# Performance work log

Hardware: AMD Instinct MI355X
Metric: run time of the kernel (lower is better)

The kernel has to match this reference:

```python
import jax, jax.numpy as jnp
import numpy as np

B, T, C = 2, 2048, 1024
H = 16
D = C // H
SCALE = 0.1 / (D ** 0.5)  # nonstandard 0.1/sqrt(head_dim) scale from source


def setup_inputs() -> dict:
    key = jax.random.key(0)
    ks = jax.random.split(key, 5)
    s = 0.02
    return {
        "x": jax.random.normal(ks[0], (B, T, C), jnp.float32),
        "w_attn": jax.random.normal(ks[1], (C, 3 * C), jnp.float32) * s,
        "b_attn": jax.random.normal(ks[2], (3 * C,), jnp.float32) * s,
        "w_proj": jax.random.normal(ks[3], (C, C), jnp.float32) * s,
        "b_proj": jax.random.normal(ks[4], (C,), jnp.float32) * s,
    }


def reference(x, w_attn, b_attn, w_proj, b_proj):
    Bs, Ts, Cs = x.shape
    qkv = x @ w_attn + b_attn                      # [B,T,3C]
    q, k, v = jnp.split(qkv, 3, axis=-1)
    q = q.reshape(Bs, Ts, H, D)                    # [B,T,H,D]
    k = k.reshape(Bs, Ts, H, D)
    v = v.reshape(Bs, Ts, H, D)
    attn = jnp.einsum("bthd,bshd->bhts", q, k) * SCALE  # [B,H,T,T]
    causal = jnp.tril(jnp.ones((Ts, Ts), dtype=bool))
    attn = jnp.where(causal, attn, -jnp.inf)
    attn = jax.nn.softmax(attn, axis=-1)
    y = jnp.einsum("bhts,bshd->bthd", attn, v).reshape(Bs, Ts, Cs)
    return y @ w_proj + b_proj
```

## Files before the change

### kernel.cpp

```cpp
#include <hip/hip_runtime.h>


#define Bz 2
#define Tz 2048
#define Cz 1024
#define Hz 16
#define Dz 64
#define QSCALE 0.01803368801111437f

typedef unsigned short u16;
typedef short bf16x4 __attribute__((ext_vector_type(4)));
typedef short bf16x8 __attribute__((ext_vector_type(8)));
typedef float f32x4 __attribute__((ext_vector_type(4)));

#define MFMA32(A, B, C) __builtin_amdgcn_mfma_f32_16x16x32_bf16(A, B, C, 0, 0, 0)

__device__ inline f32x4 mfma16(bf16x4 a, bf16x4 b, f32x4 c) {
#if defined(__HIP_DEVICE_COMPILE__)
  return __builtin_amdgcn_mfma_f32_16x16x16bf16_1k(a, b, c, 0, 0, 0);
#else
  return c;
#endif
}

__device__ inline u16 f2bf(float f) {
  return (u16)((__float_as_uint(f) + 0x8000u) >> 16);
}

__device__ inline float fexp2(float x) {
#if __has_builtin(__builtin_amdgcn_exp2f)
  return __builtin_amdgcn_exp2f(x);
#else
  return exp2f(x);
#endif
}

__device__ inline void gl_lds16(const u16* g, u16* l) {
  __builtin_amdgcn_global_load_lds(
      (const __attribute__((address_space(1))) void*)g,
      (__attribute__((address_space(3))) void*)l, 16, 0, 0);
}

#define NCAST 4096
#define NTA   3072
__global__ __launch_bounds__(256) void prep_kernel(const float* __restrict__ x,
                                                   const float* __restrict__ wa,
                                                   const float* __restrict__ wp,
                                                   u16* __restrict__ xb,
                                                   u16* __restrict__ waT,
                                                   u16* __restrict__ wpT) {
  const int bx = blockIdx.x, t = threadIdx.x;
  if (bx < NCAST) {
    int i = bx * 256 + t;
    float4 v = ((const float4*)x)[i];
    ushort4 o = {f2bf(v.x), f2bf(v.y), f2bf(v.z), f2bf(v.w)};
    ((ushort4*)xb)[i] = o;
    return;
  }
  __shared__ float tile[32][33];
  const float* W;
  u16* WT;
  int N, idx;
  if (bx < NCAST + NTA) {
    W = wa; WT = waT; N = 3 * Cz; idx = bx - NCAST;
  } else {
    W = wp; WT = wpT; N = Cz; idx = bx - NCAST - NTA;
  }
  const int n0 = (idx % (N / 32)) * 32, k0 = (idx / (N / 32)) * 32;
  const int tx = t & 31, ty = t >> 5;
#pragma unroll
  for (int i = 0; i < 4; ++i)
    tile[ty + 8 * i][tx] = W[(size_t)(k0 + ty + 8 * i) * N + n0 + tx];
  __syncthreads();
#pragma unroll
  for (int i = 0; i < 4; ++i)
    WT[(size_t)(n0 + ty + 8 * i) * Cz + k0 + tx] = f2bf(tile[tx][ty + 8 * i]);
}

template <bool OUT_BF16, int TN>
__global__ __launch_bounds__(256) void gemm_bt(const u16* __restrict__ A,
                                               const u16* __restrict__ BT,
                                               const float* __restrict__ bias,
                                               void* __restrict__ Cout,
                                               int M, int N, int K,
                                               int qcols, float qscale) {
  __shared__ __align__(16) u16 As[128 * 64];
  __shared__ __align__(16) u16 Bs[TN * 64];
  constexpr int NT = TN / 32;
  const int t = threadIdx.x;
  const int wave = t >> 6, lane = t & 63;
  const int lm = lane & 15, lg = lane >> 4;
  const int wm = wave >> 1, wn = wave & 1;
  const int m0 = blockIdx.y * 128, n0 = blockIdx.x * TN;

  const int lrow = lane >> 3;
  const int gseg = (lane & 7) ^ lrow;
  const size_t a_base = (size_t)(m0 + 32 * wave + lrow) * K + gseg * 8;
  u16* const a_lds = &As[(32 * wave) * 64];
  const size_t b_base = (size_t)(n0 + (TN / 4) * wave + lrow) * K + gseg * 8;
  u16* const b_lds = &Bs[((TN / 4) * wave) * 64];

  f32x4 acc[4][NT];
#pragma unroll
  for (int mt = 0; mt < 4; ++mt)
#pragma unroll
    for (int nt = 0; nt < NT; ++nt)
#pragma unroll
      for (int i = 0; i < 4; ++i) acc[mt][nt][i] = 0.f;

  for (int k0 = 0; k0 < K; k0 += 64) {
    __syncthreads();
#pragma unroll
    for (int i = 0; i < 4; ++i)
      gl_lds16(A + a_base + (size_t)(8 * i) * K + k0, a_lds + i * 8 * 64);
#pragma unroll
    for (int i = 0; i < NT; ++i)
      gl_lds16(BT + b_base + (size_t)(8 * i) * K + k0, b_lds + i * 8 * 64);
    __syncthreads();

#pragma unroll
    for (int h = 0; h < 2; ++h) {
      const int rs = ((lg + 4 * h) ^ (lm & 7)) * 8;
      bf16x8 af[4], bfr[NT];
#pragma unroll
      for (int mt = 0; mt < 4; ++mt)
        af[mt] = *(const bf16x8*)&As[(64 * wm + 16 * mt + lm) * 64 + rs];
#pragma unroll
      for (int nt = 0; nt < NT; ++nt)
        bfr[nt] = *(const bf16x8*)&Bs[((TN / 2) * wn + 16 * nt + lm) * 64 + rs];
#pragma unroll
      for (int mt = 0; mt < 4; ++mt)
#pragma unroll
        for (int nt = 0; nt < NT; ++nt)
          acc[mt][nt] = MFMA32(af[mt], bfr[nt], acc[mt][nt]);
    }
  }

#pragma unroll
  for (int nt = 0; nt < NT; ++nt) {
    int gc = n0 + (TN / 2) * wn + 16 * nt + lm;
    float bv = bias[gc];
    float sc = (gc < qcols) ? qscale : 1.f;
#pragma unroll
    for (int mt = 0; mt < 4; ++mt) {
#pragma unroll
      for (int i = 0; i < 4; ++i) {
        int gr = m0 + 64 * wm + 16 * mt + 4 * lg + i;
        float v = (acc[mt][nt][i] + bv) * sc;
        if (OUT_BF16)
          ((u16*)Cout)[(size_t)gr * N + gc] = f2bf(v);
        else
          ((float*)Cout)[(size_t)gr * N + gc] = v;
      }
    }
  }
}

__global__ __launch_bounds__(256) void attn_kernel(const u16* __restrict__ qkv,
                                                   u16* __restrict__ yb) {
  __shared__ __align__(16) u16 Ks[64][72];
  __shared__ __align__(16) u16 Vt[64][72];

  const int t = threadIdx.x;
  const int wave = t >> 6, lane = t & 63;
  const int lm = lane & 15, lg = lane >> 4;
  const int kg8 = lg << 3;
  const int x = blockIdx.x;
  const int bh = x & 31, qtp = x >> 5;
  const int qt = (qtp < 16) ? qtp : 47 - qtp;
  const int b = bh >> 4, h = bh & 15;
  const int q0 = qt * 64;
  const size_t rowstride = 3 * Cz;
  const u16* qbase = qkv + (size_t)b * Tz * rowstride + h * Dz;

  bf16x8 qf[2];
  {
    const u16* qrow = qbase + (size_t)(q0 + wave * 16 + lm) * rowstride + kg8;
    qf[0] = *(const bf16x8*)qrow;
    qf[1] = *(const bf16x8*)(qrow + 32);
  }

  float psum = 0.f;
  f32x4 Oa[4];
#pragma unroll
  for (int i = 0; i < 4; ++i)
#pragma unroll
    for (int j = 0; j < 4; ++j) Oa[i][j] = 0.f;

  const int ksr = t >> 2, kds = (t & 3) << 4;
  const int vsp = t & 31, vds = (t >> 5) << 3;
  const u16* kbase = qbase + Cz + (size_t)ksr * rowstride + kds;
  const u16* vbase = qbase + 2 * Cz + (size_t)(2 * vsp) * rowstride + vds;
  const size_t tilestep = 64 * rowstride;

  uint4 krA[2], vrA[2], krB[2], vrB[2];
  {
    krA[0] = *(const uint4*)kbase;
    krA[1] = *(const uint4*)(kbase + 8);
    vrA[0] = *(const uint4*)vbase;
    vrA[1] = *(const uint4*)(vbase + rowstride);
    const size_t t1 = (qt >= 1) ? tilestep : 0;
    krB[0] = *(const uint4*)(kbase + t1);
    krB[1] = *(const uint4*)(kbase + t1 + 8);
    vrB[0] = *(const uint4*)(vbase + t1);
    vrB[1] = *(const uint4*)(vbase + t1 + rowstride);
  }

  auto stage = [&](uint4 (&kr)[2], uint4 (&vr)[2], int ktc) {
    __syncthreads();
    *(uint4*)&Ks[ksr][kds] = kr[0];
    *(uint4*)&Ks[ksr][kds + 8] = kr[1];
    {
      unsigned av[4] = {vr[0].x, vr[0].y, vr[0].z, vr[0].w};
      unsigned cv[4] = {vr[1].x, vr[1].y, vr[1].z, vr[1].w};
#pragma unroll
      for (int j = 0; j < 4; ++j) {
        unsigned w0 = (av[j] & 0xffffu) | (cv[j] << 16);
        unsigned w1 = (av[j] >> 16) | (cv[j] & 0xffff0000u);
        *(unsigned*)&Vt[vds + 2 * j][2 * vsp] = w0;
        *(unsigned*)&Vt[vds + 2 * j + 1][2 * vsp] = w1;
      }
    }
    __syncthreads();

    if (ktc + 2 <= qt) {
      const u16* kp = kbase + (size_t)(ktc + 2) * tilestep;
      const u16* vp = vbase + (size_t)(ktc + 2) * tilestep;
      kr[0] = *(const uint4*)kp;
      kr[1] = *(const uint4*)(kp + 8);
      vr[0] = *(const uint4*)vp;
      vr[1] = *(const uint4*)(vp + rowstride);
    }

    f32x4 S[4];
#pragma unroll
    for (int c = 0; c < 4; ++c) {
      bf16x8 k0 = *(const bf16x8*)&Ks[c * 16 + lm][kg8];
      bf16x8 k1 = *(const bf16x8*)&Ks[c * 16 + lm][32 + kg8];
      f32x4 s;
#pragma unroll
      for (int i = 0; i < 4; ++i) s[i] = 0.f;
      s = MFMA32(k0, qf[0], s);
      s = MFMA32(k1, qf[1], s);
      S[c] = s;
    }

    const bool diag = (ktc == qt);
    const int qloc = 16 * wave + lm;
    bf16x4 pf[4];
#pragma unroll
    for (int c = 0; c < 4; ++c) {
#pragma unroll
      for (int r = 0; r < 4; ++r) {
        float p = fexp2(S[c][r]);
        if (diag && (c * 16 + 4 * lg + r) > qloc) p = 0.f;
        psum += p;
        pf[c][r] = (short)f2bf(p);
      }
    }

#pragma unroll
    for (int dt = 0; dt < 4; ++dt) {
#pragma unroll
      for (int c = 0; c < 4; ++c) {
        bf16x4 vfr = *(const bf16x4*)&Vt[16 * dt + lm][c * 16 + 4 * lg];
        Oa[dt] = mfma16(pf[c], vfr, Oa[dt]);
      }
    }
  };

  for (int kt = 0; kt <= qt; kt += 2) {
    stage(krA, vrA, kt);
    if (kt + 1 <= qt) stage(krB, vrB, kt + 1);
  }

  float s = psum;
  s += __shfl_xor(s, 16);
  s += __shfl_xor(s, 32);
  const float linv = 1.f / s;
  float invq[4];
#pragma unroll
  for (int r = 0; r < 4; ++r)
    invq[r] = __shfl(linv, 20 * lg + r);
  __syncthreads();
#pragma unroll
  for (int dt = 0; dt < 4; ++dt)
#pragma unroll
    for (int r = 0; r < 4; ++r)
      Ks[16 * wave + 4 * lg + r][16 * dt + lm] = f2bf(Oa[dt][r] * invq[r]);
  __syncthreads();
  {
    const int row = lane >> 2, seg = lane & 3;
    const uint4* src = (const uint4*)&Ks[16 * wave + row][seg * 16];
    uint4 v0 = src[0];
    uint4 v1 = src[1];
    u16* dst = yb + (size_t)(b * Tz + q0 + 16 * wave + row) * Cz + h * Dz + seg * 16;
    *(uint4*)dst = v0;
    *(uint4*)(dst + 8) = v1;
  }
}

extern "C" void kernel_launch(void* const* d_in, const int* in_sizes, int n_in,
                              void* d_out, int out_size, void* d_ws, size_t ws_size,
                              hipStream_t stream) {
  const float* x      = (const float*)d_in[0];
  const float* w_attn = (const float*)d_in[1];
  const float* b_attn = (const float*)d_in[2];
  const float* w_proj = (const float*)d_in[3];
  const float* b_proj = (const float*)d_in[4];

  char* ws = (char*)d_ws;
  u16* xb   = (u16*)(ws);
  u16* waT  = (u16*)(ws + (8ull << 20));
  u16* wpT  = (u16*)(ws + (14ull << 20));
  u16* qkvb = (u16*)(ws + (16ull << 20));
  u16* yb   = (u16*)(ws + (40ull << 20));

  const int M = Bz * Tz;

  prep_kernel<<<NCAST + NTA + 1024, 256, 0, stream>>>(x, w_attn, w_proj, xb, waT, wpT);
  gemm_bt<true, 128><<<dim3(3 * Cz / 128, M / 128), 256, 0, stream>>>(
      xb, waT, b_attn, qkvb, M, 3 * Cz, Cz, Cz, QSCALE);
  attn_kernel<<<1024, 256, 0, stream>>>(qkvb, yb);
  gemm_bt<false, 64><<<dim3(Cz / 64, M / 128), 256, 0, stream>>>(
      yb, wpT, b_proj, d_out, M, Cz, Cz, 0, 1.f);
}
```

Before: 207.9 us.

## Double-buffer K/V shared tiles to halve barriers per attention tile

The attention kernel now keeps two LDS buffers for K and transposed V. Each iteration writes the next tile into the idle buffer while computing on the current one, so it needs one barrier per tile instead of two, and global prefetch runs two tiles ahead from a single register set. The LDS row paddings also change (76 and 74 elements) to alter bank mapping. Those strides are no longer 16-byte multiples, so the vector LDS reads and writes become misaligned, which could add cost or depend on unaligned-LDS support.

```diff
diff --git a/kernel.cpp b/kernel.cpp
--- a/kernel.cpp
+++ b/kernel.cpp
@@ -7,6 +7,8 @@
 #define Hz 16
 #define Dz 64
 #define QSCALE 0.01803368801111437f
+#define KSS 76
+#define VTS 74
 
 typedef unsigned short u16;
 typedef short bf16x4 __attribute__((ext_vector_type(4)));
@@ -158,8 +160,8 @@
 
 __global__ __launch_bounds__(256) void attn_kernel(const u16* __restrict__ qkv,
                                                    u16* __restrict__ yb) {
-  __shared__ __align__(16) u16 Ks[64][72];
-  __shared__ __align__(16) u16 Vt[64][72];
+  __shared__ __align__(16) u16 Ks[2][64][KSS];
+  __shared__ __align__(16) u16 Vt[2][64][VTS];
 
   const int t = threadIdx.x;
   const int wave = t >> 6, lane = t & 63;
@@ -193,50 +195,46 @@
   const u16* vbase = qbase + 2 * Cz + (size_t)(2 * vsp) * rowstride + vds;
   const size_t tilestep = 64 * rowstride;
 
-  uint4 krA[2], vrA[2], krB[2], vrB[2];
-  {
-    krA[0] = *(const uint4*)kbase;
-    krA[1] = *(const uint4*)(kbase + 8);
-    vrA[0] = *(const uint4*)vbase;
-    vrA[1] = *(const uint4*)(vbase + rowstride);
-    const size_t t1 = (qt >= 1) ? tilestep : 0;
-    krB[0] = *(const uint4*)(kbase + t1);
-    krB[1] = *(const uint4*)(kbase + t1 + 8);
-    vrB[0] = *(const uint4*)(vbase + t1);
-    vrB[1] = *(const uint4*)(vbase + t1 + rowstride);
-  }
-
-  auto stage = [&](uint4 (&kr)[2], uint4 (&vr)[2], int ktc) {
+  uint4 kr[2], vr[2];
+  auto load_tile = [&](int kt) {
+    const u16* kp = kbase + (size_t)kt * tilestep;
+    const u16* vp = vbase + (size_t)kt * tilestep;
+    kr[0] = *(const uint4*)kp;
+    kr[1] = *(const uint4*)(kp + 8);
+    vr[0] = *(const uint4*)vp;
+    vr[1] = *(const uint4*)(vp + rowstride);
+  };
+  auto stage_write = [&](int buf) {
+    *(uint4*)&Ks[buf][ksr][kds] = kr[0];
+    *(uint4*)&Ks[buf][ksr][kds + 8] = kr[1];
+    unsigned av[4] = {vr[0].x, vr[0].y, vr[0].z, vr[0].w};
+    unsigned cv[4] = {vr[1].x, vr[1].y, vr[1].z, vr[1].w};
+#pragma unroll
+    for (int j = 0; j < 4; ++j) {
+      unsigned w0 = (av[j] & 0xffffu) | (cv[j] << 16);
+      unsigned w1 = (av[j] >> 16) | (cv[j] & 0xffff0000u);
+      *(unsigned*)&Vt[buf][vds + 2 * j][2 * vsp] = w0;
+      *(unsigned*)&Vt[buf][vds + 2 * j + 1][2 * vsp] = w1;
+    }
+  };
+
+  load_tile(0);
+  stage_write(0);
+  load_tile(1);
+
+  for (int kt = 0; kt <= qt; ++kt) {
     __syncthreads();
-    *(uint4*)&Ks[ksr][kds] = kr[0];
-    *(uint4*)&Ks[ksr][kds + 8] = kr[1];
-    {
-      unsigned av[4] = {vr[0].x, vr[0].y, vr[0].z, vr[0].w};
-      unsigned cv[4] = {vr[1].x, vr[1].y, vr[1].z, vr[1].w};
-#pragma unroll
-      for (int j = 0; j < 4; ++j) {
-        unsigned w0 = (av[j] & 0xffffu) | (cv[j] << 16);
-        unsigned w1 = (av[j] >> 16) | (cv[j] & 0xffff0000u);
-        *(unsigned*)&Vt[vds + 2 * j][2 * vsp] = w0;
-        *(unsigned*)&Vt[vds + 2 * j + 1][2 * vsp] = w1;
-      }
-    }
-    __syncthreads();
-
-    if (ktc + 2 <= qt) {
-      const u16* kp = kbase + (size_t)(ktc + 2) * tilestep;
-      const u16* vp = vbase + (size_t)(ktc + 2) * tilestep;
-      kr[0] = *(const uint4*)kp;
-      kr[1] = *(const uint4*)(kp + 8);
-      vr[0] = *(const uint4*)vp;
-      vr[1] = *(const uint4*)(vp + rowstride);
+    const int cb = kt & 1;
+    if (kt + 1 <= qt) {
+      stage_write(1 - cb);
+      if (kt + 2 <= qt) load_tile(kt + 2);
     }
 
     f32x4 S[4];
 #pragma unroll
     for (int c = 0; c < 4; ++c) {
-      bf16x8 k0 = *(const bf16x8*)&Ks[c * 16 + lm][kg8];
-      bf16x8 k1 = *(const bf16x8*)&Ks[c * 16 + lm][32 + kg8];
+      bf16x8 k0 = *(const bf16x8*)&Ks[cb][c * 16 + lm][kg8];
+      bf16x8 k1 = *(const bf16x8*)&Ks[cb][c * 16 + lm][32 + kg8];
       f32x4 s;
 #pragma unroll
       for (int i = 0; i < 4; ++i) s[i] = 0.f;
@@ -245,7 +243,7 @@
       S[c] = s;
     }
 
-    const bool diag = (ktc == qt);
+    const bool diag = (kt == qt);
     const int qloc = 16 * wave + lm;
     bf16x4 pf[4];
 #pragma unroll
@@ -263,15 +261,10 @@
     for (int dt = 0; dt < 4; ++dt) {
 #pragma unroll
       for (int c = 0; c < 4; ++c) {
-        bf16x4 vfr = *(const bf16x4*)&Vt[16 * dt + lm][c * 16 + 4 * lg];
+        bf16x4 vfr = *(const bf16x4*)&Vt[cb][16 * dt + lm][c * 16 + 4 * lg];
         Oa[dt] = mfma16(pf[c], vfr, Oa[dt]);
       }
     }
-  };
-
-  for (int kt = 0; kt <= qt; kt += 2) {
-    stage(krA, vrA, kt);
-    if (kt + 1 <= qt) stage(krB, vrB, kt + 1);
   }
 
   float s = psum;
@@ -287,11 +280,11 @@
   for (int dt = 0; dt < 4; ++dt)
 #pragma unroll
     for (int r = 0; r < 4; ++r)
-      Ks[16 * wave + 4 * lg + r][16 * dt + lm] = f2bf(Oa[dt][r] * invq[r]);
+      Ks[0][16 * wave + 4 * lg + r][16 * dt + lm] = f2bf(Oa[dt][r] * invq[r]);
   __syncthreads();
   {
     const int row = lane >> 2, seg = lane & 3;
-    const uint4* src = (const uint4*)&Ks[16 * wave + row][seg * 16];
+    const uint4* src = (const uint4*)&Ks[0][16 * wave + row][seg * 16];
     uint4 v0 = src[0];
     uint4 v1 = src[1];
     u16* dst = yb + (size_t)(b * Tz + q0 + 16 * wave + row) * Cz + h * Dz + seg * 16;
```

New measurement: 203.6 us. -2.1%, faster.
